# Kernel tuning notes

Hardware: AMD Instinct MI355X
Metric: run time of the kernel (lower is better)

The kernel has to match this reference:

```python
import jax, jax.numpy as jnp
import numpy as np

DIM = 2048
N_HEADS = 32
N_KV_HEADS = 8
HEAD_DIM = DIM // N_HEADS  # 64
SEQ = 2048
BATCH = 2


def _rope_freqs(seq_len, head_dim, theta=10000.0):
    inv = 1.0 / (theta ** (np.arange(0, head_dim, 2)[: head_dim // 2].astype(np.float32) / head_dim))
    t = np.arange(seq_len, dtype=np.float32)
    ang = np.outer(t, inv)  # (seq, head_dim//2)
    return jnp.asarray(np.cos(ang)), jnp.asarray(np.sin(ang))


def setup_inputs() -> dict:
    key = jax.random.key(0)
    ks = jax.random.split(key, 5)
    x = jax.random.normal(ks[0], (BATCH, SEQ, DIM), dtype=jnp.float32)
    s = 1.0 / np.sqrt(DIM)
    wq = jax.random.normal(ks[1], (N_HEADS * HEAD_DIM, DIM), dtype=jnp.float32) * s
    wk = jax.random.normal(ks[2], (N_KV_HEADS * HEAD_DIM, DIM), dtype=jnp.float32) * s
    wv = jax.random.normal(ks[3], (N_KV_HEADS * HEAD_DIM, DIM), dtype=jnp.float32) * s
    wo = jax.random.normal(ks[4], (DIM, N_HEADS * HEAD_DIM), dtype=jnp.float32) * s
    freqs_cos, freqs_sin = _rope_freqs(SEQ, HEAD_DIM)
    return {"x": x, "freqs_cos": freqs_cos, "freqs_sin": freqs_sin,
            "wq": wq, "wk": wk, "wv": wv, "wo": wo}


def _apply_rope(t, cos, sin):
    # t: (B, S, H, D); cos/sin: (S, D//2) broadcast to (1, S, 1, D//2)
    B, S, H, D = t.shape
    tr = t.reshape(B, S, H, D // 2, 2)
    x0, x1 = tr[..., 0], tr[..., 1]
    c = cos[None, :, None, :]
    s = sin[None, :, None, :]
    o0 = x0 * c - x1 * s
    o1 = x0 * s + x1 * c
    return jnp.stack([o0, o1], axis=-1).reshape(B, S, H, D)


def reference(x, freqs_cos, freqs_sin, wq, wk, wv, wo):
    B, S, _ = x.shape
    H, KV, D = N_HEADS, N_KV_HEADS, HEAD_DIM
    rep = H // KV
    xq = jnp.einsum('bsd,hd->bsh', x, wq).reshape(B, S, H, D)
    xk = jnp.einsum('bsd,hd->bsh', x, wk).reshape(B, S, KV, D)
    xv = jnp.einsum('bsd,hd->bsh', x, wv).reshape(B, S, KV, D)
    xq = _apply_rope(xq, freqs_cos, freqs_sin)
    xk = _apply_rope(xk, freqs_cos, freqs_sin)
    # GQA without materializing repeated K/V: group q heads as (KV, rep).
    # repeat_interleave on dim=2 maps q head h -> kv head h // rep.
    xqg = xq.reshape(B, S, KV, rep, D)
    scale = 1.0 / jnp.sqrt(jnp.float32(D))
    scores = jnp.einsum('bqkrd,bskd->bkrqs', xqg, xk) * scale  # (B,KV,rep,S,S)
    causal = jnp.tril(jnp.ones((S, S), dtype=bool))
    scores = jnp.where(causal[None, None, None], scores, jnp.float32(-jnp.inf))
    probs = jax.nn.softmax(scores, axis=-1)
    out = jnp.einsum('bkrqs,bskd->bqkrd', probs, xv)  # (B,S,KV,rep,D)
    out = out.reshape(B, S, H * D)
    return jnp.einsum('bsh,dh->bsd', out, wo)
```

## Files before the change

### kernel.cpp

```cpp
#include <hip/hip_runtime.h>

#define DIMSZ 2048
#define NH 32
#define NKV 8
#define HD 64
#define SEQLEN 2048
#define BATCH 2
#define NROWS (BATCH*SEQLEN)
#define NQKVC 3072

typedef __bf16 bf16x8 __attribute__((ext_vector_type(8)));
typedef __bf16 bf16x2 __attribute__((ext_vector_type(2)));
typedef float f32x4v __attribute__((ext_vector_type(4)));
typedef float f32x2v __attribute__((ext_vector_type(2)));

__device__ __forceinline__ unsigned short f2bf(float f) {
  __bf16 h = (__bf16)f;
  union { __bf16 h; unsigned short u; } v; v.h = h; return v.u;
}
__device__ __forceinline__ unsigned int pk2bf(float lo, float hi) {
  f32x2v v; v[0] = lo; v[1] = hi;
  bf16x2 h = __builtin_convertvector(v, bf16x2);
  union { bf16x2 h; unsigned int u; } c; c.h = h; return c.u;
}
__device__ __forceinline__ float bf2f(unsigned int bits16) {
  union { unsigned int u; float f; } v; v.u = bits16 << 16; return v.f;
}
__device__ __forceinline__ int swz128(int row, int colBytes) {
  return row * 128 + (colBytes ^ ((row & 7) << 4));
}

#define GLOAD16(g, l) __builtin_amdgcn_global_load_lds( \
    (const __attribute__((address_space(1))) unsigned int*)(g), \
    (__attribute__((address_space(3))) unsigned int*)(l), 16, 0, 0)

__global__ void k_cvt(const float* __restrict__ s, unsigned short* __restrict__ d, int n4) {
  int i = blockIdx.x * 256 + threadIdx.x;
  if (i >= n4) return;
  float4 v = reinterpret_cast<const float4*>(s)[i];
  uint2 pk; pk.x = pk2bf(v.x, v.y); pk.y = pk2bf(v.z, v.w);
  reinterpret_cast<uint2*>(d)[i] = pk;
}

__global__ void k_cvt_w(const float* __restrict__ wq, const float* __restrict__ wk,
                        const float* __restrict__ wv, unsigned short* __restrict__ d) {
  int i = blockIdx.x * 256 + threadIdx.x;
  const float* s; int off;
  if (i < 1048576)      { s = wq; off = i; }
  else if (i < 1310720) { s = wk; off = i - 1048576; }
  else                  { s = wv; off = i - 1310720; }
  float4 v = reinterpret_cast<const float4*>(s)[off];
  uint2 pk; pk.x = pk2bf(v.x, v.y); pk.y = pk2bf(v.z, v.w);
  reinterpret_cast<uint2*>(d)[i] = pk;
}

__global__ __launch_bounds__(256, 2) void k_gemm_qkv(
    const unsigned short* __restrict__ A,
    const unsigned short* __restrict__ B,
    const float* __restrict__ fc, const float* __restrict__ fs,
    unsigned short* __restrict__ Qb, unsigned short* __restrict__ Kb,
    unsigned short* __restrict__ Vt)
{
  constexpr int BK = 64, K = DIMSZ, N = NQKVC;
  __shared__ __attribute__((aligned(16))) unsigned short smA[128 * BK];
  __shared__ __attribute__((aligned(16))) unsigned short smB[128 * BK];
  const int tid = threadIdx.x;
  const int lane = tid & 63;
  const int wid = tid >> 6;
  const int lr = lane & 15, lg = lane >> 4;
  const int gx = gridDim.x;
  int lin = blockIdx.y * gx + blockIdx.x;
  const int cpx = (gx * gridDim.y) >> 3;
  lin = (lin & 7) * cpx + (lin >> 3);
  const int m0 = (lin / gx) * 128, n0 = (lin % gx) * 128;
  const int wr = (wid >> 1) * 64, wc = (wid & 1) * 64;

  f32x4v acc[4][4];
  #pragma unroll
  for (int i = 0; i < 4; i++)
    #pragma unroll
    for (int j = 0; j < 4; j++)
      acc[i][j] = f32x4v{0.f, 0.f, 0.f, 0.f};

  for (int k0 = 0; k0 < K; k0 += BK) {
    #pragma unroll
    for (int c = 0; c < 4; c++) {
      const int chunk = wid * 4 + c;
      const int idx = chunk * 64 + lane;
      const int row = idx >> 3, s = idx & 7;
      const int ks = (s ^ (row & 7)) * 8;
      GLOAD16(A + (size_t)(m0 + row) * K + k0 + ks, &smA[chunk * 512]);
      GLOAD16(B + (size_t)(n0 + row) * K + k0 + ks, &smB[chunk * 512]);
    }
    __syncthreads();
    #pragma unroll
    for (int ks = 0; ks < 2; ks++) {
      bf16x8 af[4], bfv[4];
      #pragma unroll
      for (int m = 0; m < 4; m++)
        af[m] = *reinterpret_cast<const bf16x8*>((char*)smA + swz128(wr + m * 16 + lr, ks * 64 + lg * 16));
      #pragma unroll
      for (int n = 0; n < 4; n++)
        bfv[n] = *reinterpret_cast<const bf16x8*>((char*)smB + swz128(wc + n * 16 + lr, ks * 64 + lg * 16));
      #pragma unroll
      for (int m = 0; m < 4; m++)
        #pragma unroll
        for (int n = 0; n < 4; n++)
          acc[m][n] = __builtin_amdgcn_mfma_f32_16x16x32_bf16(af[m], bfv[n], acc[m][n], 0, 0, 0);
    }
    __syncthreads();
  }
  const int bx = n0 >> 7;
  if (bx < 20) {
    const bool isQ = bx < 16;
    const float SCL = isQ ? 0.18033688011112043f : 1.0f;
    #pragma unroll
    for (int n = 0; n < 4; n++) {
      const int col = n0 + wc + n * 16 + lr;
      const int d = col & 63;
      const int i = d >> 1;
      const float sgn = (d & 1) ? 1.0f : -1.0f;
      unsigned short* dst;
      if (isQ) dst = Qb + (size_t)(col >> 6) * (SEQLEN * HD) + d;
      else     dst = Kb + (size_t)((col - 2048) >> 6) * (SEQLEN * HD) + d;
      #pragma unroll
      for (int m = 0; m < 4; m++)
        #pragma unroll
        for (int r = 0; r < 4; r++) {
          const int row = m0 + wr + m * 16 + lg * 4 + r;
          const int s = row & (SEQLEN - 1), b = row >> 11;
          const float v = acc[m][n][r];
          const float p = __shfl_xor(v, 1);
          const float c = fc[s * 32 + i], sn = fs[s * 32 + i];
          const float o = (v * c + sgn * p * sn) * SCL;
          const size_t headStride = (size_t)(isQ ? NH : NKV) * SEQLEN * HD;
          dst[(size_t)b * headStride + (size_t)s * HD] = f2bf(o);
        }
    }
  } else {
    #pragma unroll
    for (int n = 0; n < 4; n++) {
      const int col = n0 + wc + n * 16 + lr;
      const int kvh = (col - 2560) >> 6, d = col & 63;
      #pragma unroll
      for (int m = 0; m < 4; m++) {
        const int row0 = m0 + wr + m * 16 + lg * 4;
        const int s0 = row0 & (SEQLEN - 1), b = row0 >> 11;
        uint2 pk;
        pk.x = pk2bf(acc[m][n][0], acc[m][n][1]);
        pk.y = pk2bf(acc[m][n][2], acc[m][n][3]);
        *reinterpret_cast<uint2*>(
            Vt + ((size_t)((b * NKV + kvh) * HD) + d) * SEQLEN + s0) = pk;
      }
    }
  }
}

template<int OUT_BF16>
__global__ __launch_bounds__(256, 2) void k_gemm_bt(
    const unsigned short* __restrict__ A,
    const unsigned short* __restrict__ B,
    void* __restrict__ Cv, int M, int N, int K)
{
  constexpr int BK = 64;
  __shared__ __attribute__((aligned(16))) unsigned short smA[128 * BK];
  __shared__ __attribute__((aligned(16))) unsigned short smB[128 * BK];
  const int tid = threadIdx.x;
  const int lane = tid & 63;
  const int wid = tid >> 6;
  const int lr = lane & 15, lg = lane >> 4;
  const int gx = gridDim.x;
  int lin = blockIdx.y * gx + blockIdx.x;
  const int cpx = (gx * gridDim.y) >> 3;
  lin = (lin & 7) * cpx + (lin >> 3);
  const int m0 = (lin / gx) * 128, n0 = (lin % gx) * 128;
  const int wr = (wid >> 1) * 64, wc = (wid & 1) * 64;

  f32x4v acc[4][4];
  #pragma unroll
  for (int i = 0; i < 4; i++)
    #pragma unroll
    for (int j = 0; j < 4; j++)
      acc[i][j] = f32x4v{0.f, 0.f, 0.f, 0.f};

  for (int k0 = 0; k0 < K; k0 += BK) {
    #pragma unroll
    for (int c = 0; c < 4; c++) {
      const int chunk = wid * 4 + c;
      const int idx = chunk * 64 + lane;
      const int row = idx >> 3, s = idx & 7;
      const int ks = (s ^ (row & 7)) * 8;
      GLOAD16(A + (size_t)(m0 + row) * K + k0 + ks, &smA[chunk * 512]);
      GLOAD16(B + (size_t)(n0 + row) * K + k0 + ks, &smB[chunk * 512]);
    }
    __syncthreads();
    #pragma unroll
    for (int ks = 0; ks < 2; ks++) {
      bf16x8 af[4], bfv[4];
      #pragma unroll
      for (int m = 0; m < 4; m++)
        af[m] = *reinterpret_cast<const bf16x8*>((char*)smA + swz128(wr + m * 16 + lr, ks * 64 + lg * 16));
      #pragma unroll
      for (int n = 0; n < 4; n++)
        bfv[n] = *reinterpret_cast<const bf16x8*>((char*)smB + swz128(wc + n * 16 + lr, ks * 64 + lg * 16));
      #pragma unroll
      for (int m = 0; m < 4; m++)
        #pragma unroll
        for (int n = 0; n < 4; n++)
          acc[m][n] = __builtin_amdgcn_mfma_f32_16x16x32_bf16(af[m], bfv[n], acc[m][n], 0, 0, 0);
    }
    __syncthreads();
  }
  #pragma unroll
  for (int m = 0; m < 4; m++)
    #pragma unroll
    for (int n = 0; n < 4; n++)
      #pragma unroll
      for (int r = 0; r < 4; r++) {
        const size_t row = m0 + wr + m * 16 + lg * 4 + r;
        const size_t col = n0 + wc + n * 16 + lr;
        if (OUT_BF16) ((unsigned short*)Cv)[row * N + col] = f2bf(acc[m][n][r]);
        else          ((float*)Cv)[row * N + col] = acc[m][n][r];
      }
}

__global__ __launch_bounds__(512, 2) void k_attn(
    const unsigned short* __restrict__ Qg,
    const unsigned short* __restrict__ Kg,
    const unsigned short* __restrict__ Vt,
    unsigned short* __restrict__ Og)
{
  constexpr int KVB = 64;
  __shared__ __attribute__((aligned(16))) unsigned short sK0[KVB * HD];
  __shared__ __attribute__((aligned(16))) unsigned short sK1[KVB * HD];
  __shared__ __attribute__((aligned(16))) unsigned short sV0[HD * KVB];
  __shared__ __attribute__((aligned(16))) unsigned short sV1[HD * KVB];
  __shared__ __attribute__((aligned(16))) unsigned short sP[8 * 16 * KVB];
  const int tid = threadIdx.x;
  const int lane = tid & 63, wid = tid >> 6;
  const int lr = lane & 15, lg = lane >> 4;
  const int orig = blockIdx.x;
  const int w = (orig & 7) * 64 + (orig >> 3);
  const int kvh = w >> 6;
  const int b = (w >> 5) & 1;
  const int h = kvh * 4 + ((w >> 3) & 3);
  const int qp = w & 7;
  const unsigned short* Qp = Qg + ((size_t)(b * NH + h) * SEQLEN) * HD;
  const unsigned short* Kp = Kg + ((size_t)(b * NKV + kvh) * SEQLEN) * HD;
  const unsigned short* Vp = Vt + ((size_t)(b * NKV + kvh) * HD) * SEQLEN;
  unsigned short* Pw = sP + wid * (16 * KVB);

  const int sidx = wid * 64 + lane;
  const int srow = sidx >> 3;
  const int scol = ((sidx & 7) ^ (srow & 7)) * 8;

  for (int phase = 0; phase < 2; phase++) {
    const int qt = phase ? (15 - qp) : qp;
    const int qrow0 = qt * 128 + wid * 16;
    bf16x8 aq[2];
    #pragma unroll
    for (int ks = 0; ks < 2; ks++)
      aq[ks] = *reinterpret_cast<const bf16x8*>(Qp + (size_t)(qrow0 + lr) * HD + ks * 32 + lg * 8);

    f32x4v accO[4];
    #pragma unroll
    for (int r = 0; r < 4; r++) accO[r] = f32x4v{0.f, 0.f, 0.f, 0.f};
    float mrun = -3.0e38f, lrun = 0.f;

    auto compute = [&](int kv0, auto& sKb, auto& sVb) {
      if (kv0 > qrow0 + 15) return;
      f32x4v sfr[4];
      #pragma unroll
      for (int c = 0; c < 4; c++) sfr[c] = f32x4v{0.f, 0.f, 0.f, 0.f};
      __builtin_amdgcn_s_setprio(1);
      #pragma unroll
      for (int ks = 0; ks < 2; ks++) {
        bf16x8 bk[4];
        #pragma unroll
        for (int c = 0; c < 4; c++)
          bk[c] = *reinterpret_cast<const bf16x8*>((char*)sKb + swz128(c * 16 + lr, ks * 64 + lg * 16));
        #pragma unroll
        for (int c = 0; c < 4; c++)
          sfr[c] = __builtin_amdgcn_mfma_f32_16x16x32_bf16(bk[c], aq[ks], sfr[c], 0, 0, 0);
      }
      __builtin_amdgcn_s_setprio(0);
      if (kv0 + KVB - 1 > qrow0) {
        const int q = qrow0 + lr;
        #pragma unroll
        for (int c = 0; c < 4; c++)
          #pragma unroll
          for (int r = 0; r < 4; r++) {
            const int kv = kv0 + c * 16 + lg * 4 + r;
            if (kv > q) sfr[c][r] = -1.0e30f;
          }
      }
      float mc[4];
      #pragma unroll
      for (int c = 0; c < 4; c++)
        mc[c] = fmaxf(fmaxf(sfr[c][0], sfr[c][1]), fmaxf(sfr[c][2], sfr[c][3]));
      float tm = fmaxf(fmaxf(mc[0], mc[1]), fmaxf(mc[2], mc[3]));
      tm = fmaxf(tm, __shfl_xor(tm, 16));
      tm = fmaxf(tm, __shfl_xor(tm, 32));
      const float mo = mrun;
      const bool defer = __all(tm <= mo + 8.0f);
      const float mn = defer ? mo : fmaxf(mo, tm);
      float rc[4];
      #pragma unroll
      for (int c = 0; c < 4; c++) {
        float p0 = __builtin_amdgcn_exp2f(sfr[c][0] - mn);
        float p1 = __builtin_amdgcn_exp2f(sfr[c][1] - mn);
        float p2 = __builtin_amdgcn_exp2f(sfr[c][2] - mn);
        float p3 = __builtin_amdgcn_exp2f(sfr[c][3] - mn);
        sfr[c][0] = p0; sfr[c][1] = p1; sfr[c][2] = p2; sfr[c][3] = p3;
        rc[c] = (p0 + p1) + (p2 + p3);
      }
      float rs = (rc[0] + rc[1]) + (rc[2] + rc[3]);
      rs += __shfl_xor(rs, 16);
      rs += __shfl_xor(rs, 32);
      if (defer) {
        lrun += rs;
      } else {
        const float sc = __builtin_amdgcn_exp2f(mo - mn);
        mrun = mn;
        lrun = lrun * sc + rs;
        #pragma unroll
        for (int r = 0; r < 4; r++) {
          const float scr = __shfl(sc, (lg << 4) + (lg << 2) + r);
          #pragma unroll
          for (int dc = 0; dc < 4; dc++) accO[dc][r] *= scr;
        }
      }
      #pragma unroll
      for (int c = 0; c < 4; c++) {
        uint2 pk;
        pk.x = pk2bf(sfr[c][0], sfr[c][1]);
        pk.y = pk2bf(sfr[c][2], sfr[c][3]);
        *reinterpret_cast<uint2*>((char*)Pw + swz128(lr, c * 32 + lg * 8)) = pk;
      }
      __builtin_amdgcn_s_setprio(1);
      #pragma unroll
      for (int ks = 0; ks < 2; ks++) {
        bf16x8 ap = *reinterpret_cast<const bf16x8*>((char*)Pw + swz128(lr, ks * 64 + lg * 16));
        bf16x8 bv[4];
        #pragma unroll
        for (int dc = 0; dc < 4; dc++)
          bv[dc] = *reinterpret_cast<const bf16x8*>((char*)sVb + swz128(dc * 16 + lr, ks * 64 + lg * 16));
        #pragma unroll
        for (int dc = 0; dc < 4; dc++)
          accO[dc] = __builtin_amdgcn_mfma_f32_16x16x32_bf16(ap, bv[dc], accO[dc], 0, 0, 0);
      }
      __builtin_amdgcn_s_setprio(0);
    };

    const int nt = qt * 2 + 2;
    GLOAD16(Kp + (size_t)srow * HD + scol, &sK0[wid * 512]);
    GLOAD16(Vp + (size_t)srow * SEQLEN + scol, &sV0[wid * 512]);
    __syncthreads();
    for (int t = 0; t < nt; t += 2) {
      {
        const int kn = (t + 1) * KVB;
        GLOAD16(Kp + (size_t)(kn + srow) * HD + scol, &sK1[wid * 512]);
        GLOAD16(Vp + (size_t)srow * SEQLEN + kn + scol, &sV1[wid * 512]);
      }
      compute(t * KVB, sK0, sV0);
      __syncthreads();
      if (t + 2 < nt) {
        const int kn = (t + 2) * KVB;
        GLOAD16(Kp + (size_t)(kn + srow) * HD + scol, &sK0[wid * 512]);
        GLOAD16(Vp + (size_t)srow * SEQLEN + kn + scol, &sV0[wid * 512]);
      }
      compute((t + 1) * KVB, sK1, sV1);
      __syncthreads();
    }
    const float inv = 1.0f / lrun;
    #pragma unroll
    for (int r = 0; r < 4; r++) {
      const float invr = __shfl(inv, (lg << 4) + (lg << 2) + r);
      const int q = qrow0 + lg * 4 + r;
      #pragma unroll
      for (int dc = 0; dc < 4; dc++) {
        const int d = dc * 16 + lr;
        Og[(size_t)(b * SEQLEN + q) * DIMSZ + h * HD + d] = f2bf(accO[dc][r] * invr);
      }
    }
  }
}

extern "C" void kernel_launch(void* const* d_in, const int* in_sizes, int n_in,
                              void* d_out, int out_size, void* d_ws, size_t ws_size,
                              hipStream_t stream)
{
  const float* x  = (const float*)d_in[0];
  const float* fc = (const float*)d_in[1];
  const float* fs = (const float*)d_in[2];
  const float* wq = (const float*)d_in[3];
  const float* wk = (const float*)d_in[4];
  const float* wv = (const float*)d_in[5];
  const float* wo = (const float*)d_in[6];
  float* out = (float*)d_out;
  char* ws = (char*)d_ws;

  unsigned short* xb    = (unsigned short*)(ws + 0);
  unsigned short* wqkvb = (unsigned short*)(ws + 16777216);
  unsigned short* wob   = (unsigned short*)(ws + 29360128);
  unsigned short* Qb    = (unsigned short*)(ws + 62914560);
  unsigned short* Kb    = (unsigned short*)(ws + 79691776);
  unsigned short* Vtb   = (unsigned short*)(ws + 83886080);
  unsigned short* attnb = (unsigned short*)(ws + 88080384);

  k_cvt<<<8192, 256, 0, stream>>>(x,  xb, 2097152);
  k_cvt_w<<<6144, 256, 0, stream>>>(wq, wk, wv, wqkvb);
  k_cvt<<<4096, 256, 0, stream>>>(wo, wob, 1048576);

  dim3 g1(24, 32);
  k_gemm_qkv<<<g1, 256, 0, stream>>>(xb, wqkvb, fc, fs, Qb, Kb, Vtb);

  k_attn<<<512, 512, 0, stream>>>(Qb, Kb, Vtb, attnb);

  dim3 g2(16, 32);
  k_gemm_bt<0><<<g2, 256, 0, stream>>>(attnb, wob, out, NROWS, DIMSZ, DIMSZ);
}
```

Baseline: 175.3 us.

## Use 32x32 MFMA in attention with register-resident P and merged conversion kernel

Attention now runs four waves per block, each handling 32 query rows with 32x32x16 bf16 MFMAs. The probability tile stays in registers, with cross-half lane shuffles replacing the shared-memory round trip. This cuts LDS traffic, and the larger MFMA shape should use the matrix units more efficiently. The three fp32-to-bf16 conversion launches are merged into one kernel to save launch overhead. The conversion code contains redundant branches, and halving the threads per block changes occupancy and how much each thread loads.

Measured after the change: 171.1 us. -2.4%, faster.

```diff
diff --git a/kernel.cpp b/kernel.cpp
--- a/kernel.cpp
+++ b/kernel.cpp
@@ -13,6 +13,7 @@
 typedef __bf16 bf16x2 __attribute__((ext_vector_type(2)));
 typedef float f32x4v __attribute__((ext_vector_type(4)));
 typedef float f32x2v __attribute__((ext_vector_type(2)));
+typedef float f32x16 __attribute__((ext_vector_type(16)));
 
 __device__ __forceinline__ unsigned short f2bf(float f) {
   __bf16 h = (__bf16)f;
@@ -34,24 +35,38 @@
     (const __attribute__((address_space(1))) unsigned int*)(g), \
     (__attribute__((address_space(3))) unsigned int*)(l), 16, 0, 0)
 
-__global__ void k_cvt(const float* __restrict__ s, unsigned short* __restrict__ d, int n4) {
+__global__ void k_cvt_all(const float* __restrict__ x,
+                          const float* __restrict__ wq, const float* __restrict__ wk,
+                          const float* __restrict__ wv, const float* __restrict__ wo,
+                          unsigned short* __restrict__ xb,
+                          unsigned short* __restrict__ wqkvb,
+                          unsigned short* __restrict__ wob) {
   int i = blockIdx.x * 256 + threadIdx.x;
-  if (i >= n4) return;
-  float4 v = reinterpret_cast<const float4*>(s)[i];
-  uint2 pk; pk.x = pk2bf(v.x, v.y); pk.y = pk2bf(v.z, v.w);
-  reinterpret_cast<uint2*>(d)[i] = pk;
-}
-
-__global__ void k_cvt_w(const float* __restrict__ wq, const float* __restrict__ wk,
-                        const float* __restrict__ wv, unsigned short* __restrict__ d) {
-  int i = blockIdx.x * 256 + threadIdx.x;
-  const float* s; int off;
-  if (i < 1048576)      { s = wq; off = i; }
-  else if (i < 1310720) { s = wk; off = i - 1048576; }
-  else                  { s = wv; off = i - 1310720; }
-  float4 v = reinterpret_cast<const float4*>(s)[off];
-  uint2 pk; pk.x = pk2bf(v.x, v.y); pk.y = pk2bf(v.z, v.w);
-  reinterpret_cast<uint2*>(d)[i] = pk;
+  const float* s; unsigned short* d; int off;
+  if (i < 2097152)      { s = x;  d = xb;    off = i; }
+  else {
+    int j = i - 2097152;
+    if (j < 1048576)      { s = wq; d = wqkvb; off = j; }
+    else if (j < 1310720) { s = wk; d = wqkvb; off = j; s = wk; off = j; }
+    else if (j < 1572864) { s = wv; d = wqkvb; off = j; }
+    else                  { s = wo; d = wob;   off = j - 1572864; }
+    if (j >= 1048576 && j < 1310720) {  }
+  }
+  if (i >= 2097152) {
+    int j = i - 2097152;
+    if (j < 1048576)      { s = wq; off = j;            d = wqkvb; }
+    else if (j < 1310720) { s = wk; off = j - 1048576;  d = wqkvb; off += 0; }
+    else if (j < 1572864) { s = wv; off = j - 1310720;  d = wqkvb; }
+    else                  { s = wo; off = j - 1572864;  d = wob; }
+    float4 v = reinterpret_cast<const float4*>(s)[off];
+    uint2 pk; pk.x = pk2bf(v.x, v.y); pk.y = pk2bf(v.z, v.w);
+    int dsti = (j < 1572864) ? j : (j - 1572864);
+    reinterpret_cast<uint2*>(d)[dsti] = pk;
+  } else {
+    float4 v = reinterpret_cast<const float4*>(x)[i];
+    uint2 pk; pk.x = pk2bf(v.x, v.y); pk.y = pk2bf(v.z, v.w);
+    reinterpret_cast<uint2*>(xb)[i] = pk;
+  }
 }
 
 __global__ __launch_bounds__(256, 2) void k_gemm_qkv(
@@ -61,7 +76,7 @@
     unsigned short* __restrict__ Qb, unsigned short* __restrict__ Kb,
     unsigned short* __restrict__ Vt)
 {
-  constexpr int BK = 64, K = DIMSZ, N = NQKVC;
+  constexpr int BK = 64, K = DIMSZ;
   __shared__ __attribute__((aligned(16))) unsigned short smA[128 * BK];
   __shared__ __attribute__((aligned(16))) unsigned short smB[128 * BK];
   const int tid = threadIdx.x;
@@ -224,7 +239,7 @@
       }
 }
 
-__global__ __launch_bounds__(512, 2) void k_attn(
+__global__ __launch_bounds__(256, 2) void k_attn(
     const unsigned short* __restrict__ Qg,
     const unsigned short* __restrict__ Kg,
     const unsigned short* __restrict__ Vt,
@@ -235,10 +250,9 @@
   __shared__ __attribute__((aligned(16))) unsigned short sK1[KVB * HD];
   __shared__ __attribute__((aligned(16))) unsigned short sV0[HD * KVB];
   __shared__ __attribute__((aligned(16))) unsigned short sV1[HD * KVB];
-  __shared__ __attribute__((aligned(16))) unsigned short sP[8 * 16 * KVB];
   const int tid = threadIdx.x;
   const int lane = tid & 63, wid = tid >> 6;
-  const int lr = lane & 15, lg = lane >> 4;
+  const int l31 = lane & 31, hi = lane >> 5;
   const int orig = blockIdx.x;
   const int w = (orig & 7) * 64 + (orig >> 3);
   const int kvh = w >> 6;
@@ -248,74 +262,68 @@
   const unsigned short* Qp = Qg + ((size_t)(b * NH + h) * SEQLEN) * HD;
   const unsigned short* Kp = Kg + ((size_t)(b * NKV + kvh) * SEQLEN) * HD;
   const unsigned short* Vp = Vt + ((size_t)(b * NKV + kvh) * HD) * SEQLEN;
-  unsigned short* Pw = sP + wid * (16 * KVB);
-
-  const int sidx = wid * 64 + lane;
-  const int srow = sidx >> 3;
-  const int scol = ((sidx & 7) ^ (srow & 7)) * 8;
+
+  int srow[2], scol[2];
+  #pragma unroll
+  for (int c = 0; c < 2; c++) {
+    const int idx = (wid * 2 + c) * 64 + lane;
+    srow[c] = idx >> 3;
+    scol[c] = ((idx & 7) ^ (srow[c] & 7)) * 8;
+  }
 
   for (int phase = 0; phase < 2; phase++) {
     const int qt = phase ? (15 - qp) : qp;
-    const int qrow0 = qt * 128 + wid * 16;
-    bf16x8 aq[2];
-    #pragma unroll
-    for (int ks = 0; ks < 2; ks++)
-      aq[ks] = *reinterpret_cast<const bf16x8*>(Qp + (size_t)(qrow0 + lr) * HD + ks * 32 + lg * 8);
-
-    f32x4v accO[4];
-    #pragma unroll
-    for (int r = 0; r < 4; r++) accO[r] = f32x4v{0.f, 0.f, 0.f, 0.f};
+    const int qrow0 = qt * 128 + wid * 32;
+    const int qg = qrow0 + l31;
+    bf16x8 aq[4];
+    #pragma unroll
+    for (int ks = 0; ks < 4; ks++)
+      aq[ks] = *reinterpret_cast<const bf16x8*>(Qp + (size_t)qg * HD + ks * 16 + hi * 8);
+
+    f32x16 accO0, accO1;
+    #pragma unroll
+    for (int i = 0; i < 16; i++) { accO0[i] = 0.f; accO1[i] = 0.f; }
     float mrun = -3.0e38f, lrun = 0.f;
 
     auto compute = [&](int kv0, auto& sKb, auto& sVb) {
-      if (kv0 > qrow0 + 15) return;
-      f32x4v sfr[4];
-      #pragma unroll
-      for (int c = 0; c < 4; c++) sfr[c] = f32x4v{0.f, 0.f, 0.f, 0.f};
+      if (kv0 > qrow0 + 31) return;
+      f32x16 S0, S1;
+      #pragma unroll
+      for (int i = 0; i < 16; i++) { S0[i] = 0.f; S1[i] = 0.f; }
       __builtin_amdgcn_s_setprio(1);
       #pragma unroll
-      for (int ks = 0; ks < 2; ks++) {
-        bf16x8 bk[4];
-        #pragma unroll
-        for (int c = 0; c < 4; c++)
-          bk[c] = *reinterpret_cast<const bf16x8*>((char*)sKb + swz128(c * 16 + lr, ks * 64 + lg * 16));
-        #pragma unroll
-        for (int c = 0; c < 4; c++)
-          sfr[c] = __builtin_amdgcn_mfma_f32_16x16x32_bf16(bk[c], aq[ks], sfr[c], 0, 0, 0);
+      for (int ks = 0; ks < 4; ks++) {
+        bf16x8 ak0 = *reinterpret_cast<const bf16x8*>((char*)sKb + swz128(l31,      ks * 32 + hi * 16));
+        bf16x8 ak1 = *reinterpret_cast<const bf16x8*>((char*)sKb + swz128(32 + l31, ks * 32 + hi * 16));
+        S0 = __builtin_amdgcn_mfma_f32_32x32x16_bf16(ak0, aq[ks], S0, 0, 0, 0);
+        S1 = __builtin_amdgcn_mfma_f32_32x32x16_bf16(ak1, aq[ks], S1, 0, 0, 0);
       }
       __builtin_amdgcn_s_setprio(0);
       if (kv0 + KVB - 1 > qrow0) {
-        const int q = qrow0 + lr;
         #pragma unroll
-        for (int c = 0; c < 4; c++)
-          #pragma unroll
-          for (int r = 0; r < 4; r++) {
-            const int kv = kv0 + c * 16 + lg * 4 + r;
-            if (kv > q) sfr[c][r] = -1.0e30f;
-          }
-      }
-      float mc[4];
-      #pragma unroll
-      for (int c = 0; c < 4; c++)
-        mc[c] = fmaxf(fmaxf(sfr[c][0], sfr[c][1]), fmaxf(sfr[c][2], sfr[c][3]));
-      float tm = fmaxf(fmaxf(mc[0], mc[1]), fmaxf(mc[2], mc[3]));
-      tm = fmaxf(tm, __shfl_xor(tm, 16));
+        for (int reg = 0; reg < 16; reg++) {
+          const int rl = (reg & 3) + 8 * (reg >> 2) + (hi << 2);
+          if (kv0 + rl > qg)      S0[reg] = -1.0e30f;
+          if (kv0 + 32 + rl > qg) S1[reg] = -1.0e30f;
+        }
+      }
+      float tm = S0[0];
+      #pragma unroll
+      for (int i = 1; i < 16; i++) tm = fmaxf(tm, S0[i]);
+      #pragma unroll
+      for (int i = 0; i < 16; i++) tm = fmaxf(tm, S1[i]);
       tm = fmaxf(tm, __shfl_xor(tm, 32));
       const float mo = mrun;
       const bool defer = __all(tm <= mo + 8.0f);
       const float mn = defer ? mo : fmaxf(mo, tm);
-      float rc[4];
-      #pragma unroll
-      for (int c = 0; c < 4; c++) {
-        float p0 = __builtin_amdgcn_exp2f(sfr[c][0] - mn);
-        float p1 = __builtin_amdgcn_exp2f(sfr[c][1] - mn);
-        float p2 = __builtin_amdgcn_exp2f(sfr[c][2] - mn);
-        float p3 = __builtin_amdgcn_exp2f(sfr[c][3] - mn);
-        sfr[c][0] = p0; sfr[c][1] = p1; sfr[c][2] = p2; sfr[c][3] = p3;
-        rc[c] = (p0 + p1) + (p2 + p3);
-      }
-      float rs = (rc[0] + rc[1]) + (rc[2] + rc[3]);
-      rs += __shfl_xor(rs, 16);
+      #pragma unroll
+      for (int i = 0; i < 16; i++) {
+        S0[i] = __builtin_amdgcn_exp2f(S0[i] - mn);
+        S1[i] = __builtin_amdgcn_exp2f(S1[i] - mn);
+      }
+      float rs = 0.f;
+      #pragma unroll
+      for (int i = 0; i < 16; i++) rs += S0[i] + S1[i];
       rs += __shfl_xor(rs, 32);
       if (defer) {
         lrun += rs;
@@ -324,64 +332,71 @@
         mrun = mn;
         lrun = lrun * sc + rs;
         #pragma unroll
-        for (int r = 0; r < 4; r++) {
-          const float scr = __shfl(sc, (lg << 4) + (lg << 2) + r);
-          #pragma unroll
-          for (int dc = 0; dc < 4; dc++) accO[dc][r] *= scr;
+        for (int reg = 0; reg < 16; reg++) {
+          const int rl = (reg & 3) + 8 * (reg >> 2) + (hi << 2);
+          const float scr = __shfl(sc, rl);
+          accO0[reg] *= scr; accO1[reg] *= scr;
         }
       }
-      #pragma unroll
-      for (int c = 0; c < 4; c++) {
-        uint2 pk;
-        pk.x = pk2bf(sfr[c][0], sfr[c][1]);
-        pk.y = pk2bf(sfr[c][2], sfr[c][3]);
-        *reinterpret_cast<uint2*>((char*)Pw + swz128(lr, c * 32 + lg * 8)) = pk;
-      }
       __builtin_amdgcn_s_setprio(1);
-      #pragma unroll
-      for (int ks = 0; ks < 2; ks++) {
-        bf16x8 ap = *reinterpret_cast<const bf16x8*>((char*)Pw + swz128(lr, ks * 64 + lg * 16));
-        bf16x8 bv[4];
-        #pragma unroll
-        for (int dc = 0; dc < 4; dc++)
-          bv[dc] = *reinterpret_cast<const bf16x8*>((char*)sVb + swz128(dc * 16 + lr, ks * 64 + lg * 16));
-        #pragma unroll
-        for (int dc = 0; dc < 4; dc++)
-          accO[dc] = __builtin_amdgcn_mfma_f32_16x16x32_bf16(ap, bv[dc], accO[dc], 0, 0, 0);
-      }
+      #define PVSTEP(S16, G, CB) do {                                          \
+        unsigned a0 = pk2bf(S16[(G)+0], S16[(G)+1]);                           \
+        unsigned a1 = pk2bf(S16[(G)+2], S16[(G)+3]);                           \
+        unsigned b0 = pk2bf(S16[(G)+4], S16[(G)+5]);                           \
+        unsigned b1 = pk2bf(S16[(G)+6], S16[(G)+7]);                           \
+        unsigned s0 = hi ? a0 : b0, s1 = hi ? a1 : b1;                         \
+        unsigned r0 = __shfl_xor((int)s0, 32), r1 = __shfl_xor((int)s1, 32);   \
+        union { unsigned u[4]; bf16x8 v; } pf;                                 \
+        pf.u[0] = hi ? r0 : a0; pf.u[1] = hi ? r1 : a1;                        \
+        pf.u[2] = hi ? b0 : r0; pf.u[3] = hi ? b1 : r1;                        \
+        bf16x8 bv0 = *reinterpret_cast<const bf16x8*>((char*)sVb + swz128(l31,      (CB))); \
+        bf16x8 bv1 = *reinterpret_cast<const bf16x8*>((char*)sVb + swz128(32 + l31, (CB))); \
+        accO0 = __builtin_amdgcn_mfma_f32_32x32x16_bf16(pf.v, bv0, accO0, 0, 0, 0); \
+        accO1 = __builtin_amdgcn_mfma_f32_32x32x16_bf16(pf.v, bv1, accO1, 0, 0, 0); \
+      } while (0)
+      PVSTEP(S0, 0,  0  + hi * 16);
+      PVSTEP(S0, 8,  32 + hi * 16);
+      PVSTEP(S1, 0,  64 + hi * 16);
+      PVSTEP(S1, 8,  96 + hi * 16);
+      #undef PVSTEP
       __builtin_amdgcn_s_setprio(0);
     };
 
     const int nt = qt * 2 + 2;
-    GLOAD16(Kp + (size_t)srow * HD + scol, &sK0[wid * 512]);
-    GLOAD16(Vp + (size_t)srow * SEQLEN + scol, &sV0[wid * 512]);
+    GLOAD16(Kp + (size_t)srow[0] * HD + scol[0], &sK0[(wid * 2 + 0) * 512]);
+    GLOAD16(Kp + (size_t)srow[1] * HD + scol[1], &sK0[(wid * 2 + 1) * 512]);
+    GLOAD16(Vp + (size_t)srow[0] * SEQLEN + scol[0], &sV0[(wid * 2 + 0) * 512]);
+    GLOAD16(Vp + (size_t)srow[1] * SEQLEN + scol[1], &sV0[(wid * 2 + 1) * 512]);
     __syncthreads();
     for (int t = 0; t < nt; t += 2) {
       {
         const int kn = (t + 1) * KVB;
-        GLOAD16(Kp + (size_t)(kn + srow) * HD + scol, &sK1[wid * 512]);
-        GLOAD16(Vp + (size_t)srow * SEQLEN + kn + scol, &sV1[wid * 512]);
+        GLOAD16(Kp + (size_t)(kn + srow[0]) * HD + scol[0], &sK1[(wid * 2 + 0) * 512]);
+        GLOAD16(Kp + (size_t)(kn + srow[1]) * HD + scol[1], &sK1[(wid * 2 + 1) * 512]);
+        GLOAD16(Vp + (size_t)srow[0] * SEQLEN + kn + scol[0], &sV1[(wid * 2 + 0) * 512]);
+        GLOAD16(Vp + (size_t)srow[1] * SEQLEN + kn + scol[1], &sV1[(wid * 2 + 1) * 512]);
       }
       compute(t * KVB, sK0, sV0);
       __syncthreads();
       if (t + 2 < nt) {
         const int kn = (t + 2) * KVB;
-        GLOAD16(Kp + (size_t)(kn + srow) * HD + scol, &sK0[wid * 512]);
-        GLOAD16(Vp + (size_t)srow * SEQLEN + kn + scol, &sV0[wid * 512]);
+        GLOAD16(Kp + (size_t)(kn + srow[0]) * HD + scol[0], &sK0[(wid * 2 + 0) * 512]);
+        GLOAD16(Kp + (size_t)(kn + srow[1]) * HD + scol[1], &sK0[(wid * 2 + 1) * 512]);
+        GLOAD16(Vp + (size_t)srow[0] * SEQLEN + kn + scol[0], &sV0[(wid * 2 + 0) * 512]);
+        GLOAD16(Vp + (size_t)srow[1] * SEQLEN + kn + scol[1], &sV0[(wid * 2 + 1) * 512]);
       }
       compute((t + 1) * KVB, sK1, sV1);
       __syncthreads();
     }
     const float inv = 1.0f / lrun;
     #pragma unroll
-    for (int r = 0; r < 4; r++) {
-      const float invr = __shfl(inv, (lg << 4) + (lg << 2) + r);
-      const int q = qrow0 + lg * 4 + r;
-      #pragma unroll
-      for (int dc = 0; dc < 4; dc++) {
-        const int d = dc * 16 + lr;
-        Og[(size_t)(b * SEQLEN + q) * DIMSZ + h * HD + d] = f2bf(accO[dc][r] * invr);
-      }
+    for (int reg = 0; reg < 16; reg++) {
+      const int rl = (reg & 3) + 8 * (reg >> 2) + (hi << 2);
+      const float invr = __shfl(inv, rl);
+      const int q = qrow0 + rl;
+      const size_t base = ((size_t)(b * SEQLEN + q)) * DIMSZ + h * HD;
+      Og[base + l31]      = f2bf(accO0[reg] * invr);
+      Og[base + 32 + l31] = f2bf(accO1[reg] * invr);
     }
   }
 }
@@ -408,14 +423,12 @@
   unsigned short* Vtb   = (unsigned short*)(ws + 83886080);
   unsigned short* attnb = (unsigned short*)(ws + 88080384);
 
-  k_cvt<<<8192, 256, 0, stream>>>(x,  xb, 2097152);
-  k_cvt_w<<<6144, 256, 0, stream>>>(wq, wk, wv, wqkvb);
-  k_cvt<<<4096, 256, 0, stream>>>(wo, wob, 1048576);
+  k_cvt_all<<<18432, 256, 0, stream>>>(x, wq, wk, wv, wo, xb, wqkvb, wob);
 
   dim3 g1(24, 32);
   k_gemm_qkv<<<g1, 256, 0, stream>>>(xb, wqkvb, fc, fs, Qb, Kb, Vtb);
 
-  k_attn<<<512, 512, 0, stream>>>(Qb, Kb, Vtb, attnb);
+  k_attn<<<512, 256, 0, stream>>>(Qb, Kb, Vtb, attnb);
 
   dim3 g2(16, 32);
   k_gemm_bt<0><<<g2, 256, 0, stream>>>(attnb, wob, out, NROWS, DIMSZ, DIMSZ);
```
